# Kernel optimization log

Measured on AMD Instinct MI355X. Metric: run time of the kernel, lower is better.

Reference implementation:

```python
import jax, jax.numpy as jnp
import numpy as np

N_NODES = 100000
N_EDGES = 1600000
D_IN = 128
D_HID = 128
N_CLS = 16
N_GRAPHS = 64


def setup_inputs() -> dict:
    key = jax.random.key(0)
    ks = jax.random.split(key, 12)
    h = jax.random.normal(ks[0], (N_NODES, D_IN), dtype=jnp.float32)
    src = jax.random.randint(ks[1], (N_EDGES,), 0, N_NODES, dtype=jnp.int32)
    dst = jax.random.randint(ks[2], (N_EDGES,), 0, N_NODES, dtype=jnp.int32)
    graph_ids = jnp.sort(jax.random.randint(ks[3], (N_NODES,), 0, N_GRAPHS, dtype=jnp.int32))
    s = 1.0 / np.sqrt(D_IN)
    W1_self = jax.random.uniform(ks[4], (D_IN, D_HID), jnp.float32, -s, s)
    W1_neigh = jax.random.uniform(ks[5], (D_IN, D_HID), jnp.float32, -s, s)
    b1 = jnp.zeros((D_HID,), jnp.float32)
    s2 = 1.0 / np.sqrt(D_HID)
    W2_self = jax.random.uniform(ks[6], (D_HID, D_HID), jnp.float32, -s2, s2)
    W2_neigh = jax.random.uniform(ks[7], (D_HID, D_HID), jnp.float32, -s2, s2)
    b2 = jnp.zeros((D_HID,), jnp.float32)
    Wc = jax.random.uniform(ks[8], (D_HID, N_CLS), jnp.float32, -s2, s2)
    bc = jnp.zeros((N_CLS,), jnp.float32)
    return {"h": h, "src": src, "dst": dst, "graph_ids": graph_ids, "num_graphs": N_GRAPHS,
            "W1_self": W1_self, "W1_neigh": W1_neigh, "b1": b1,
            "W2_self": W2_self, "W2_neigh": W2_neigh, "b2": b2,
            "Wc": Wc, "bc": bc}


def _sage_conv(h, src, dst, W_self, W_neigh, b):
    # DGL SAGEConv 'mean': out = fc_self(h) + fc_neigh(mean of in-neighbor feats) + bias
    n = h.shape[0]
    msg = jnp.take(h, src, axis=0)                               # [E, d] gather
    agg = jax.ops.segment_sum(msg, dst, num_segments=n)          # [N, d] scatter-add
    deg = jax.ops.segment_sum(jnp.ones((src.shape[0],), h.dtype), dst, num_segments=n)
    neigh = agg / jnp.maximum(deg, 1.0)[:, None]                 # mean, zero-degree safe
    return h @ W_self + neigh @ W_neigh + b


def reference(h, src, dst, graph_ids, num_graphs,
              W1_self, W1_neigh, b1, W2_self, W2_neigh, b2, Wc, bc):
    x = jax.nn.relu(_sage_conv(h, src, dst, W1_self, W1_neigh, b1))
    x = _sage_conv(x, src, dst, W2_self, W2_neigh, b2)
    # dgl.mean_nodes: per-graph mean over node features
    gsum = jax.ops.segment_sum(x, graph_ids, num_segments=num_graphs)    # [G, d]
    gcnt = jax.ops.segment_sum(jnp.ones((x.shape[0],), x.dtype), graph_ids, num_segments=num_graphs)
    hg = gsum / jnp.maximum(gcnt, 1.0)[:, None]
    return hg @ Wc + bc                                                  # [G, num_classes]
```

## Files before the change

kernel.cpp:

```cpp
#include <hip/hip_runtime.h>

#define D        128
#define N_GRAPHS 64
#define N_CLS    16
#define LDA      40
#define SLOTS    48
#define CAP      8192

typedef unsigned int   uint;
typedef unsigned short ushort;
typedef __attribute__((ext_vector_type(8))) short short8;
typedef __attribute__((ext_vector_type(4))) float f32x4;

__device__ inline ushort f2b(float f) {
    uint u = __float_as_uint(f);
    u += 0x7fffu + ((u >> 16) & 1u);
    return (ushort)(u >> 16);
}

__device__ __forceinline__ int swz2i(int row, int col) {
    return row * 256 + (col ^ (((row ^ (row >> 3)) & 7) << 3));
}


__global__ __launch_bounds__(256) void k_boot(
    const float* __restrict__ h, ushort* __restrict__ fb,
    const float* __restrict__ Ws, const float* __restrict__ Wn,
    ushort* __restrict__ wT,
    const int* __restrict__ gid, int* __restrict__ gstart,
    const int* __restrict__ src, const int* __restrict__ dst,
    int* __restrict__ bcount, uint* __restrict__ ebuf,
    int E, int NB, int N, int t4) {
    __shared__ int hist[512], base[512], lcur[512];
    int bb = blockIdx.x;
    int t  = threadIdx.x;

    if (bb < 256) {
        int per = (E + 255) / 256;
        int e0 = bb * per;
        int e1 = min(e0 + per, E);
        for (int i = t; i < NB; i += 256) { hist[i] = 0; lcur[i] = 0; }
        __syncthreads();
        for (int e = e0 + t; e < e1; e += 256) atomicAdd(&hist[dst[e] >> 8], 1);
        __syncthreads();
        for (int i = t; i < NB; i += 256)
            base[i] = hist[i] ? atomicAdd(&bcount[i], hist[i]) : 0;
        __syncthreads();
        for (int e = e0 + t; e < e1; e += 256) {
            int dd = dst[e];
            int b = dd >> 8;
            int off = atomicAdd(&lcur[b], 1);
            int pos = base[b] + off;
            if (pos < CAP)
                ebuf[(size_t)b * CAP + pos] = ((uint)src[e] << 8) | (uint)(dd & 255);
        }
    } else if (bb < 384) {
        int i = (bb - 256) * 256 + t;
        int c = i >> 8, k = i & 255;
        float v = (k < 128) ? Ws[k * 128 + c] : Wn[(k - 128) * 128 + c];
        wT[c * 256 + k] = f2b(v);
    } else if (bb == 384) {
        int g = t;
        if (g <= N_GRAPHS) {
            int lo = 0, hi = N;
            while (lo < hi) {
                int mid = (lo + hi) >> 1;
                if (gid[mid] < g) lo = mid + 1; else hi = mid;
            }
            gstart[g] = lo;
        }
    } else {
        int i = (bb - 385) * 256 + t;
        if (i < t4) {
            float4 v = ((const float4*)h)[i];
            ushort4 o;
            o.x = f2b(v.x); o.y = f2b(v.y); o.z = f2b(v.z); o.w = f2b(v.w);
            ((ushort4*)fb)[i] = o;
        }
    }
}


__global__ __launch_bounds__(1024) void k_bucket(
    const uint* __restrict__ ebuf, const int* __restrict__ bcount,
    int* __restrict__ csrf, int* __restrict__ deg, float* __restrict__ invdeg,
    int N) {
    __shared__ int ldeg[256];
    __shared__ int lcsr[256 * SLOTS];
    int b = blockIdx.x, t = threadIdx.x;
    if (t < 256) ldeg[t] = 0;
    __syncthreads();
    int cnt = bcount[b];
    if (cnt > CAP) cnt = CAP;
    const uint* __restrict__ eb = ebuf + (size_t)b * CAP;
    for (int i = t; i < cnt; i += 1024) {
        uint r = eb[i];
        int dl = r & 255;
        int sl = atomicAdd(&ldeg[dl], 1);
        if (sl < SLOTS) lcsr[dl * SLOTS + sl] = (int)(r >> 8);
    }
    __syncthreads();
    int n0 = b << 8;
    int lim = (N - n0) * SLOTS;
    if (lim > 256 * SLOTS) lim = 256 * SLOTS;
    for (int i = t; i < lim; i += 1024)
        csrf[(size_t)n0 * SLOTS + i] = lcsr[i];
    if (t < 256 && n0 + t < N) {
        int d = ldeg[t];
        deg[n0 + t] = d;
        invdeg[n0 + t] = 1.0f / (float)(d > 1 ? d : 1);
    }
}


__global__ __launch_bounds__(256) void k_agp(
    const ushort* __restrict__ fb, const int* __restrict__ deg,
    const int* __restrict__ csrf, const float* __restrict__ invdeg,
    ushort* __restrict__ outb, int N, int AB,
    const int* __restrict__ src, const int* __restrict__ dst,
    const int* __restrict__ gid,
    int* __restrict__ bcount2, uint* __restrict__ ebuf2, int E, int NB) {
    __shared__ int hist[512], base[512], lcur[512];

    if (blockIdx.x >= AB) {
        int bb = blockIdx.x - AB;
        int t = threadIdx.x;
        int per = (E + 255) / 256;
        int e0 = bb * per;
        int e1 = min(e0 + per, E);
        for (int i = t; i < NB; i += 256) { hist[i] = 0; lcur[i] = 0; }
        __syncthreads();
        for (int e = e0 + t; e < e1; e += 256) atomicAdd(&hist[src[e] >> 8], 1);
        __syncthreads();
        for (int i = t; i < NB; i += 256)
            base[i] = hist[i] ? atomicAdd(&bcount2[i], hist[i]) : 0;
        __syncthreads();
        for (int e = e0 + t; e < e1; e += 256) {
            int ss = src[e];
            int dd = dst[e];
            int bk = ss >> 8;
            int off = atomicAdd(&lcur[bk], 1);
            int pos = base[bk] + off;
            if (pos < CAP) {
                int g  = gid[dd];
                int dc = deg[dd]; if (dc > 127) dc = 127;
                ebuf2[(size_t)bk * CAP + pos] =
                    (uint)(ss & 255) | ((uint)g << 8) | ((uint)dc << 14);
            }
        }
        return;
    }

    int lane = threadIdx.x & 63;
    int n = blockIdx.x * 4 + (threadIdx.x >> 6);
    if (n >= N) return;
    int d = deg[n];
    if (d > SLOTS) d = SLOTS;
    const int* __restrict__ lst = csrf + (size_t)n * SLOTS;
    int ej = lane >> 4;
    int cg = lane & 15;

    float acc[8];
#pragma unroll
    for (int i = 0; i < 8; i++) acc[i] = 0.f;

    int e = ej;
    for (; e + 4 < d; e += 8) {
        int s0 = lst[e];
        int s1 = lst[e + 4];
        uint4 v0 = *(const uint4*)(fb + (size_t)s0 * D + cg * 8);
        uint4 v1 = *(const uint4*)(fb + (size_t)s1 * D + cg * 8);
        acc[0] += __uint_as_float(v0.x << 16);
        acc[1] += __uint_as_float(v0.x & 0xffff0000u);
        acc[2] += __uint_as_float(v0.y << 16);
        acc[3] += __uint_as_float(v0.y & 0xffff0000u);
        acc[4] += __uint_as_float(v0.z << 16);
        acc[5] += __uint_as_float(v0.z & 0xffff0000u);
        acc[6] += __uint_as_float(v0.w << 16);
        acc[7] += __uint_as_float(v0.w & 0xffff0000u);
        acc[0] += __uint_as_float(v1.x << 16);
        acc[1] += __uint_as_float(v1.x & 0xffff0000u);
        acc[2] += __uint_as_float(v1.y << 16);
        acc[3] += __uint_as_float(v1.y & 0xffff0000u);
        acc[4] += __uint_as_float(v1.z << 16);
        acc[5] += __uint_as_float(v1.z & 0xffff0000u);
        acc[6] += __uint_as_float(v1.w << 16);
        acc[7] += __uint_as_float(v1.w & 0xffff0000u);
    }
    for (; e < d; e += 4) {
        int s = lst[e];
        uint4 v = *(const uint4*)(fb + (size_t)s * D + cg * 8);
        acc[0] += __uint_as_float(v.x << 16);
        acc[1] += __uint_as_float(v.x & 0xffff0000u);
        acc[2] += __uint_as_float(v.y << 16);
        acc[3] += __uint_as_float(v.y & 0xffff0000u);
        acc[4] += __uint_as_float(v.z << 16);
        acc[5] += __uint_as_float(v.z & 0xffff0000u);
        acc[6] += __uint_as_float(v.w << 16);
        acc[7] += __uint_as_float(v.w & 0xffff0000u);
    }
#pragma unroll
    for (int i = 0; i < 8; i++) {
        acc[i] += __shfl_xor(acc[i], 16);
        acc[i] += __shfl_xor(acc[i], 32);
    }
    if (ej == 0) {
        float id = invdeg[n];
        uint4 o;
        o.x = (uint)f2b(acc[0] * id) | ((uint)f2b(acc[1] * id) << 16);
        o.y = (uint)f2b(acc[2] * id) | ((uint)f2b(acc[3] * id) << 16);
        o.z = (uint)f2b(acc[4] * id) | ((uint)f2b(acc[5] * id) << 16);
        o.w = (uint)f2b(acc[6] * id) | ((uint)f2b(acc[7] * id) << 16);
        *(uint4*)(outb + (size_t)n * D + cg * 8) = o;
    }
}

__global__ __launch_bounds__(256) void k_part2s(
    const int* __restrict__ src, const int* __restrict__ dst,
    const int* __restrict__ gid, const int* __restrict__ deg,
    int* __restrict__ bcount2, uint* __restrict__ ebuf2, int E, int NB) {
    __shared__ int hist[512], base[512], lcur[512];
    int t = threadIdx.x;
    int per = (E + 255) / 256;
    int e0 = blockIdx.x * per;
    int e1 = min(e0 + per, E);
    for (int i = t; i < NB; i += 256) { hist[i] = 0; lcur[i] = 0; }
    __syncthreads();
    for (int e = e0 + t; e < e1; e += 256) atomicAdd(&hist[src[e] >> 8], 1);
    __syncthreads();
    for (int i = t; i < NB; i += 256)
        base[i] = hist[i] ? atomicAdd(&bcount2[i], hist[i]) : 0;
    __syncthreads();
    for (int e = e0 + t; e < e1; e += 256) {
        int ss = src[e];
        int dd = dst[e];
        int bk = ss >> 8;
        int off = atomicAdd(&lcur[bk], 1);
        int pos = base[bk] + off;
        if (pos < CAP) {
            int g  = gid[dd];
            int dc = deg[dd]; if (dc > 127) dc = 127;
            ebuf2[(size_t)bk * CAP + pos] =
                (uint)(ss & 255) | ((uint)g << 8) | ((uint)dc << 14);
        }
    }
}


__global__ __launch_bounds__(256, 2) void k_mm1m(
    const ushort* __restrict__ hb, const ushort* __restrict__ nbb,
    const ushort* __restrict__ wT, const float* __restrict__ b,
    ushort* __restrict__ x1b, int N) {
    __shared__ __align__(16) ushort As[128 * LDA];
    __shared__ __align__(16) ushort Bs[128 * LDA];
    int t    = threadIdx.x;
    int w    = t >> 6;
    int lane = t & 63;
    int m    = lane & 15;
    int quad = lane >> 4;
    int n0   = blockIdx.x * 128;

    f32x4 acc[2][8];
#pragma unroll
    for (int rt = 0; rt < 2; rt++)
#pragma unroll
        for (int ct = 0; ct < 8; ct++) acc[rt][ct] = (f32x4){0.f, 0.f, 0.f, 0.f};

#pragma unroll 1
    for (int kc = 0; kc < 8; kc++) {
        int k0 = kc * 32;
        const ushort* __restrict__ A = (k0 < 128) ? hb : nbb;
        int ka = k0 & 127;
        __syncthreads();
#pragma unroll
        for (int i = 0; i < 2; i++) {
            int linear = i * 256 + t;
            int row = linear >> 2;
            int q   = linear & 3;
            int nn = n0 + row;
            uint4 v = make_uint4(0u, 0u, 0u, 0u);
            if (nn < N) v = *(const uint4*)(A + (size_t)nn * D + ka + q * 8);
            *(uint4*)(&As[row * LDA + q * 8]) = v;
        }
#pragma unroll
        for (int i = 0; i < 2; i++) {
            int linear = i * 256 + t;
            int col = linear >> 2;
            int q   = linear & 3;
            uint4 v = *(const uint4*)(wT + (size_t)col * 256 + k0 + q * 8);
            *(uint4*)(&Bs[col * LDA + q * 8]) = v;
        }
        __syncthreads();
        short8 af[2], bf[8];
#pragma unroll
        for (int rt = 0; rt < 2; rt++)
            af[rt] = *(const short8*)(&As[(w * 32 + rt * 16 + m) * LDA + quad * 8]);
#pragma unroll
        for (int ct = 0; ct < 8; ct++)
            bf[ct] = *(const short8*)(&Bs[(ct * 16 + m) * LDA + quad * 8]);
#pragma unroll
        for (int rt = 0; rt < 2; rt++)
#pragma unroll
            for (int ct = 0; ct < 8; ct++)
                acc[rt][ct] = __builtin_amdgcn_mfma_f32_16x16x32_bf16(
                    af[rt], bf[ct], acc[rt][ct], 0, 0, 0);
    }
#pragma unroll
    for (int ct = 0; ct < 8; ct++) {
        float bias = b[ct * 16 + m];
#pragma unroll
        for (int rt = 0; rt < 2; rt++) {
#pragma unroll
            for (int r = 0; r < 4; r++) {
                int n = n0 + w * 32 + rt * 16 + quad * 4 + r;
                if (n < N)
                    x1b[(size_t)n * D + ct * 16 + m] =
                        f2b(fmaxf(acc[rt][ct][r] + bias, 0.f));
            }
        }
    }
}


__global__ __launch_bounds__(1024, 4) void k_wg(
    const uint* __restrict__ ebuf2, const int* __restrict__ bcount2,
    const ushort* __restrict__ x1b, const int* __restrict__ gstart,
    float* __restrict__ S1, float* __restrict__ P, int N, int WSB) {
    __shared__ __align__(16) char smem[131072];

    if (blockIdx.x >= WSB) {
        int b2 = blockIdx.x - WSB;
        int g  = b2 >> 1;
        int ch = b2 & 1;
        int r0 = gstart[g], r1 = gstart[g + 1];
        int len = r1 - r0;
        if (len <= 0) return;
        int L = (len + 1) >> 1;
        int a = r0 + ch * L;
        int bnd = min(a + L, r1);
        if (a >= bnd) return;
        int rp = threadIdx.x >> 6;
        int cp = threadIdx.x & 63;
        float ax = 0.f, ay = 0.f;
        const uint* __restrict__ M = (const uint*)x1b;
        for (int n = a + rp; n < bnd; n += 16) {
            uint v = M[(size_t)n * 64 + cp];
            ax += __uint_as_float(v << 16);
            ay += __uint_as_float(v & 0xffff0000u);
        }
        atomicAdd(&S1[g * D + cp * 2], ax);
        atomicAdd(&S1[g * D + cp * 2 + 1], ay);
        return;
    }

    float*  lwcT = (float*)smem;
    ushort* lxT  = (ushort*)smem;
    ushort* lwcb = (ushort*)(smem + 65536);
    ushort* lwlo = (ushort*)(smem + 98304);

    int b = blockIdx.x, t = threadIdx.x;
    int n0 = b << 8;

    for (int i = t; i < 16384; i += 1024) lwcT[i] = 0.f;
    __syncthreads();

    int cnt = bcount2[b];
    if (cnt > CAP) cnt = CAP;
    const uint* __restrict__ eb = ebuf2 + (size_t)b * CAP;
    for (int i = t; i < cnt; i += 1024) {
        uint r = eb[i];
        int sl = (int)(r & 255u);
        int g  = (int)((r >> 8) & 63u);
        int dc = (int)((r >> 14) & 127u);
        float id = 1.0f / (float)(dc > 1 ? dc : 1);
        atomicAdd(&lwcT[g * 256 + sl], id);
    }
    __syncthreads();

    for (int i = t; i < 16384; i += 1024) {
        int g = i >> 8, sl = i & 255;
        float v = lwcT[i];
        ushort hi = f2b(v);
        float fhi = __uint_as_float((uint)hi << 16);
        ushort lo = f2b(v - fhi);
        int si = swz2i(g, sl);
        lwcb[si] = hi;
        lwlo[si] = lo;
    }
    __syncthreads();

    const uint4* __restrict__ x4 = (const uint4*)x1b;
#pragma unroll 1
    for (int it = 0; it < 4; ++it) {
        int l = it * 1024 + t;
        int n = l >> 4, q = l & 15;
        uint4 v = make_uint4(0u, 0u, 0u, 0u);
        int nn = n0 + n;
        if (nn < N) v = x4[(size_t)nn * 16 + q];
        int d0 = q * 8;
        lxT[swz2i(d0 + 0, n)] = (ushort)(v.x & 0xffffu);
        lxT[swz2i(d0 + 1, n)] = (ushort)(v.x >> 16);
        lxT[swz2i(d0 + 2, n)] = (ushort)(v.y & 0xffffu);
        lxT[swz2i(d0 + 3, n)] = (ushort)(v.y >> 16);
        lxT[swz2i(d0 + 4, n)] = (ushort)(v.z & 0xffffu);
        lxT[swz2i(d0 + 5, n)] = (ushort)(v.z >> 16);
        lxT[swz2i(d0 + 6, n)] = (ushort)(v.w & 0xffffu);
        lxT[swz2i(d0 + 7, n)] = (ushort)(v.w >> 16);
    }
    __syncthreads();

    int wv = t >> 6, lane = t & 63, m = lane & 15, quad = lane >> 4;
    int s  = wv & 3;
    int hs = wv >> 2;
    f32x4 acc[2];
    acc[0] = (f32x4){0.f, 0.f, 0.f, 0.f};
    acc[1] = (f32x4){0.f, 0.f, 0.f, 0.f};

#pragma unroll 1
    for (int k8 = 0; k8 < 8; ++k8) {
        int kc = k8 * 32 + quad * 8;
        int ar = s * 16 + m;
        short8 ahi = *(const short8*)&lwcb[swz2i(ar, kc)];
        short8 alo = *(const short8*)&lwlo[swz2i(ar, kc)];
#pragma unroll
        for (int d2 = 0; d2 < 2; ++d2) {
            short8 bfr = *(const short8*)&lxT[swz2i(hs * 32 + d2 * 16 + m, kc)];
            acc[d2] = __builtin_amdgcn_mfma_f32_16x16x32_bf16(alo, bfr, acc[d2], 0, 0, 0);
            acc[d2] = __builtin_amdgcn_mfma_f32_16x16x32_bf16(ahi, bfr, acc[d2], 0, 0, 0);
        }
    }
    float* __restrict__ Pb = P + (size_t)b * 8192;
#pragma unroll
    for (int d2 = 0; d2 < 2; ++d2) {
#pragma unroll
        for (int r = 0; r < 4; ++r) {
            int g = s * 16 + quad * 4 + r;
            Pb[g * 128 + hs * 32 + d2 * 16 + m] = acc[d2][r];
        }
    }
}


__global__ __launch_bounds__(256) void k_final(
    const float* __restrict__ S1, const float* __restrict__ P, int NBLK,
    const int* __restrict__ gstart, const float* __restrict__ W2s,
    const float* __restrict__ W2n, const float* __restrict__ b2,
    const float* __restrict__ Wc, const float* __restrict__ bc,
    float* __restrict__ out) {
    __shared__ float s1[D], s2[2][D], hg[D];
    int g = blockIdx.x, t = threadIdx.x;
    int c = t & 127, hh = t >> 7;
    const float* __restrict__ Pg = P + (size_t)g * 128 + c;
    float a0 = 0.f, a1 = 0.f, a2 = 0.f, a3 = 0.f;
    int bb = hh;
    for (; bb + 6 < NBLK; bb += 8) {
        a0 += Pg[(size_t)bb * 8192];
        a1 += Pg[(size_t)(bb + 2) * 8192];
        a2 += Pg[(size_t)(bb + 4) * 8192];
        a3 += Pg[(size_t)(bb + 6) * 8192];
    }
    for (; bb < NBLK; bb += 2) a0 += Pg[(size_t)bb * 8192];
    s2[hh][c] = a0 + a1 + a2 + a3;
    if (hh == 0) s1[c] = S1[g * D + c];
    __syncthreads();
    if (t < 128) s2[0][c] += s2[1][c];
    __syncthreads();
    if (t < 128) {
        float acc = 0.f;
#pragma unroll 8
        for (int k = 0; k < D; k++) {
            acc = fmaf(s1[k], W2s[k * D + c], acc);
            acc = fmaf(s2[0][k], W2n[k * D + c], acc);
        }
        int cnt = gstart[g + 1] - gstart[g];
        hg[c] = (cnt > 0) ? (acc / (float)cnt + b2[c]) : 0.f;
    }
    __syncthreads();
    if (t < N_CLS) {
        float o = bc[t];
        for (int k = 0; k < D; k++) o = fmaf(hg[k], Wc[k * N_CLS + t], o);
        out[g * N_CLS + t] = o;
    }
}


extern "C" void kernel_launch(void* const* d_in, const int* in_sizes, int n_in,
                              void* d_out, int out_size, void* d_ws, size_t ws_size,
                              hipStream_t stream) {
    const float* h   = (const float*)d_in[0];
    const int*   src = (const int*)d_in[1];
    const int*   dst = (const int*)d_in[2];
    const int*   gid = (const int*)d_in[3];
    const float* W1s = (const float*)d_in[5];
    const float* W1n = (const float*)d_in[6];
    const float* b1  = (const float*)d_in[7];
    const float* W2s = (const float*)d_in[8];
    const float* W2n = (const float*)d_in[9];
    const float* b2  = (const float*)d_in[10];
    const float* Wc  = (const float*)d_in[11];
    const float* bc  = (const float*)d_in[12];
    float* out = (float*)d_out;

    const int N = in_sizes[0] / D;
    const int E = in_sizes[1];
    const int NB = (N + 255) >> 8;

    char* w = (char*)d_ws;
    size_t off = 0;
    auto alloc = [&](size_t elems) -> void* {
        void* p = w + off;
        off += elems * 4;
        return p;
    };
    float* S1      = (float*)alloc((size_t)N_GRAPHS * D);
    int*   bcount  = (int*)alloc(512);
    int*   bcount2 = (int*)alloc(512);
    size_t zero_bytes = off;
    int*   deg    = (int*)alloc(N);
    float* invdeg = (float*)alloc(N);
    int*   gstart = (int*)alloc(128);
    int*   csrf   = (int*)alloc((size_t)N * SLOTS);
    ushort* fb    = (ushort*)alloc((size_t)N * 64);
    ushort* nbb   = (ushort*)alloc((size_t)N * 64);
    ushort* x1b   = (ushort*)alloc((size_t)N * 64);
    ushort* wT    = (ushort*)alloc(16384);
    uint*  ebuf = (uint*)nbb;
    float* P    = (float*)fb;

    size_t ebuf2_units = (size_t)NB * CAP;
    bool dedicated = (off + ebuf2_units * 4) <= ws_size;
    uint* ebuf2 = dedicated ? (uint*)alloc(ebuf2_units) : (uint*)csrf;

    hipMemsetAsync(d_ws, 0, zero_bytes, stream);

    int t4 = N * 32;
    int CB = (t4 + 255) / 256;
    int MMB = (N + 127) / 128;
    int AB  = (N + 3) / 4;

    k_boot<<<256 + 128 + 1 + CB, 256, 0, stream>>>(
        h, fb, W1s, W1n, wT, gid, gstart, src, dst, bcount, ebuf, E, NB, N, t4);
    k_bucket<<<NB, 1024, 0, stream>>>(ebuf, bcount, csrf, deg, invdeg, N);
    k_agp<<<AB + (dedicated ? 256 : 0), 256, 0, stream>>>(
        fb, deg, csrf, invdeg, nbb, N, AB,
        src, dst, gid, bcount2, ebuf2, E, NB);
    if (!dedicated)
        k_part2s<<<256, 256, 0, stream>>>(src, dst, gid, deg, bcount2, ebuf2, E, NB);
    k_mm1m<<<MMB, 256, 0, stream>>>(fb, nbb, wT, b1, x1b, N);
    k_wg<<<NB + 128, 1024, 0, stream>>>(
        ebuf2, bcount2, x1b, gstart, S1, P, N, NB);
    k_final<<<N_GRAPHS, 256, 0, stream>>>(
        S1, P, NB, gstart, W2s, W2n, b2, Wc, bc, out);
}
```

Baseline: 353.7 us.

## Move source-bucket partition into boot kernel and look up graph/invdeg via packed table

The second edge partition (bucketing by src) moves out of the aggregation kernel and into the boot kernel, so it runs alongside the dst partition and no longer depends on degrees. Each bucket entry now stores the full dst index instead of a precomputed graph id and clamped degree. The bucket kernel writes a packed (graph id, inverse degree) table, which the weighting kernel gathers per edge. This frees the aggregation kernel of the partition work. In exchange the weighting kernel does a random 8-byte gather per edge, and it now uses the exact inverse degree rather than one clamped at 127.

```diff
diff --git a/kernel.cpp b/kernel.cpp
--- a/kernel.cpp
+++ b/kernel.cpp
@@ -30,6 +30,7 @@
     const int* __restrict__ gid, int* __restrict__ gstart,
     const int* __restrict__ src, const int* __restrict__ dst,
     int* __restrict__ bcount, uint* __restrict__ ebuf,
+    int* __restrict__ bcount2, uint* __restrict__ ebuf2, int doP2,
     int E, int NB, int N, int t4) {
     __shared__ int hist[512], base[512], lcur[512];
     int bb = blockIdx.x;
@@ -54,12 +55,34 @@
             if (pos < CAP)
                 ebuf[(size_t)b * CAP + pos] = ((uint)src[e] << 8) | (uint)(dd & 255);
         }
-    } else if (bb < 384) {
-        int i = (bb - 256) * 256 + t;
+    } else if (bb < 512) {
+        if (!doP2) return;
+        int bb2 = bb - 256;
+        int per = (E + 255) / 256;
+        int e0 = bb2 * per;
+        int e1 = min(e0 + per, E);
+        for (int i = t; i < NB; i += 256) { hist[i] = 0; lcur[i] = 0; }
+        __syncthreads();
+        for (int e = e0 + t; e < e1; e += 256) atomicAdd(&hist[src[e] >> 8], 1);
+        __syncthreads();
+        for (int i = t; i < NB; i += 256)
+            base[i] = hist[i] ? atomicAdd(&bcount2[i], hist[i]) : 0;
+        __syncthreads();
+        for (int e = e0 + t; e < e1; e += 256) {
+            int ss = src[e];
+            int bk = ss >> 8;
+            int off = atomicAdd(&lcur[bk], 1);
+            int pos = base[bk] + off;
+            if (pos < CAP)
+                ebuf2[(size_t)bk * CAP + pos] =
+                    ((uint)dst[e] << 8) | (uint)(ss & 255);
+        }
+    } else if (bb < 640) {
+        int i = (bb - 512) * 256 + t;
         int c = i >> 8, k = i & 255;
         float v = (k < 128) ? Ws[k * 128 + c] : Wn[(k - 128) * 128 + c];
         wT[c * 256 + k] = f2b(v);
-    } else if (bb == 384) {
+    } else if (bb == 640) {
         int g = t;
         if (g <= N_GRAPHS) {
             int lo = 0, hi = N;
@@ -70,7 +93,7 @@
             gstart[g] = lo;
         }
     } else {
-        int i = (bb - 385) * 256 + t;
+        int i = (bb - 641) * 256 + t;
         if (i < t4) {
             float4 v = ((const float4*)h)[i];
             ushort4 o;
@@ -83,8 +106,9 @@
 
 __global__ __launch_bounds__(1024) void k_bucket(
     const uint* __restrict__ ebuf, const int* __restrict__ bcount,
+    const int* __restrict__ gid,
     int* __restrict__ csrf, int* __restrict__ deg, float* __restrict__ invdeg,
-    int N) {
+    uint2* __restrict__ gipack, int N) {
     __shared__ int ldeg[256];
     __shared__ int lcsr[256 * SLOTS];
     int b = blockIdx.x, t = threadIdx.x;
@@ -108,49 +132,17 @@
     if (t < 256 && n0 + t < N) {
         int d = ldeg[t];
         deg[n0 + t] = d;
-        invdeg[n0 + t] = 1.0f / (float)(d > 1 ? d : 1);
-    }
-}
-
-
-__global__ __launch_bounds__(256) void k_agp(
+        float iv = 1.0f / (float)(d > 1 ? d : 1);
+        invdeg[n0 + t] = iv;
+        gipack[n0 + t] = make_uint2((uint)gid[n0 + t], __float_as_uint(iv));
+    }
+}
+
+
+__global__ __launch_bounds__(256) void k_aggb(
     const ushort* __restrict__ fb, const int* __restrict__ deg,
     const int* __restrict__ csrf, const float* __restrict__ invdeg,
-    ushort* __restrict__ outb, int N, int AB,
-    const int* __restrict__ src, const int* __restrict__ dst,
-    const int* __restrict__ gid,
-    int* __restrict__ bcount2, uint* __restrict__ ebuf2, int E, int NB) {
-    __shared__ int hist[512], base[512], lcur[512];
-
-    if (blockIdx.x >= AB) {
-        int bb = blockIdx.x - AB;
-        int t = threadIdx.x;
-        int per = (E + 255) / 256;
-        int e0 = bb * per;
-        int e1 = min(e0 + per, E);
-        for (int i = t; i < NB; i += 256) { hist[i] = 0; lcur[i] = 0; }
-        __syncthreads();
-        for (int e = e0 + t; e < e1; e += 256) atomicAdd(&hist[src[e] >> 8], 1);
-        __syncthreads();
-        for (int i = t; i < NB; i += 256)
-            base[i] = hist[i] ? atomicAdd(&bcount2[i], hist[i]) : 0;
-        __syncthreads();
-        for (int e = e0 + t; e < e1; e += 256) {
-            int ss = src[e];
-            int dd = dst[e];
-            int bk = ss >> 8;
-            int off = atomicAdd(&lcur[bk], 1);
-            int pos = base[bk] + off;
-            if (pos < CAP) {
-                int g  = gid[dd];
-                int dc = deg[dd]; if (dc > 127) dc = 127;
-                ebuf2[(size_t)bk * CAP + pos] =
-                    (uint)(ss & 255) | ((uint)g << 8) | ((uint)dc << 14);
-            }
-        }
-        return;
-    }
-
+    ushort* __restrict__ outb, int N) {
     int lane = threadIdx.x & 63;
     int n = blockIdx.x * 4 + (threadIdx.x >> 6);
     if (n >= N) return;
@@ -217,7 +209,6 @@
 
 __global__ __launch_bounds__(256) void k_part2s(
     const int* __restrict__ src, const int* __restrict__ dst,
-    const int* __restrict__ gid, const int* __restrict__ deg,
     int* __restrict__ bcount2, uint* __restrict__ ebuf2, int E, int NB) {
     __shared__ int hist[512], base[512], lcur[512];
     int t = threadIdx.x;
@@ -233,16 +224,11 @@
     __syncthreads();
     for (int e = e0 + t; e < e1; e += 256) {
         int ss = src[e];
-        int dd = dst[e];
         int bk = ss >> 8;
         int off = atomicAdd(&lcur[bk], 1);
         int pos = base[bk] + off;
-        if (pos < CAP) {
-            int g  = gid[dd];
-            int dc = deg[dd]; if (dc > 127) dc = 127;
-            ebuf2[(size_t)bk * CAP + pos] =
-                (uint)(ss & 255) | ((uint)g << 8) | ((uint)dc << 14);
-        }
+        if (pos < CAP)
+            ebuf2[(size_t)bk * CAP + pos] = ((uint)dst[e] << 8) | (uint)(ss & 255);
     }
 }
 
@@ -324,6 +310,7 @@
 
 __global__ __launch_bounds__(1024, 4) void k_wg(
     const uint* __restrict__ ebuf2, const int* __restrict__ bcount2,
+    const uint2* __restrict__ gipack,
     const ushort* __restrict__ x1b, const int* __restrict__ gstart,
     float* __restrict__ S1, float* __restrict__ P, int N, int WSB) {
     __shared__ __align__(16) char smem[131072];
@@ -369,11 +356,10 @@
     const uint* __restrict__ eb = ebuf2 + (size_t)b * CAP;
     for (int i = t; i < cnt; i += 1024) {
         uint r = eb[i];
+        int dn = (int)(r >> 8);
         int sl = (int)(r & 255u);
-        int g  = (int)((r >> 8) & 63u);
-        int dc = (int)((r >> 14) & 127u);
-        float id = 1.0f / (float)(dc > 1 ? dc : 1);
-        atomicAdd(&lwcT[g * 256 + sl], id);
+        uint2 gi = gipack[dn];
+        atomicAdd(&lwcT[gi.x * 256 + sl], __uint_as_float(gi.y));
     }
     __syncthreads();
 
@@ -518,6 +504,7 @@
     size_t zero_bytes = off;
     int*   deg    = (int*)alloc(N);
     float* invdeg = (float*)alloc(N);
+    uint2* gipack = (uint2*)alloc((size_t)N * 2);
     int*   gstart = (int*)alloc(128);
     int*   csrf   = (int*)alloc((size_t)N * SLOTS);
     ushort* fb    = (ushort*)alloc((size_t)N * 64);
@@ -538,17 +525,16 @@
     int MMB = (N + 127) / 128;
     int AB  = (N + 3) / 4;
 
-    k_boot<<<256 + 128 + 1 + CB, 256, 0, stream>>>(
-        h, fb, W1s, W1n, wT, gid, gstart, src, dst, bcount, ebuf, E, NB, N, t4);
-    k_bucket<<<NB, 1024, 0, stream>>>(ebuf, bcount, csrf, deg, invdeg, N);
-    k_agp<<<AB + (dedicated ? 256 : 0), 256, 0, stream>>>(
-        fb, deg, csrf, invdeg, nbb, N, AB,
-        src, dst, gid, bcount2, ebuf2, E, NB);
+    k_boot<<<641 + CB, 256, 0, stream>>>(
+        h, fb, W1s, W1n, wT, gid, gstart, src, dst,
+        bcount, ebuf, bcount2, ebuf2, dedicated ? 1 : 0, E, NB, N, t4);
+    k_bucket<<<NB, 1024, 0, stream>>>(ebuf, bcount, gid, csrf, deg, invdeg, gipack, N);
+    k_aggb<<<AB, 256, 0, stream>>>(fb, deg, csrf, invdeg, nbb, N);
     if (!dedicated)
-        k_part2s<<<256, 256, 0, stream>>>(src, dst, gid, deg, bcount2, ebuf2, E, NB);
+        k_part2s<<<256, 256, 0, stream>>>(src, dst, bcount2, ebuf2, E, NB);
     k_mm1m<<<MMB, 256, 0, stream>>>(fb, nbb, wT, b1, x1b, N);
     k_wg<<<NB + 128, 1024, 0, stream>>>(
-        ebuf2, bcount2, x1b, gstart, S1, P, N, NB);
+        ebuf2, bcount2, gipack, x1b, gstart, S1, P, N, NB);
     k_final<<<N_GRAPHS, 256, 0, stream>>>(
         S1, P, NB, gstart, W2s, W2n, b2, Wc, bc, out);
 }
```

Measured after the change: 308.8 us. 12.7% less time.
